# Performance work log

Measured on AMD Instinct MI355X. Metric: run time of the kernel, lower is better.

The kernel has to match this reference:

```python
import jax, jax.numpy as jnp
import numpy as np

# ---- static lookup-point config (matches cfg.radius/stride/level) ----
RADIUS = [4, 4, 4, 4]
STRIDE = [1, 1, 1, 1]
LEVEL = [0, 1, 2, 3]

def _build_pts():
    pts = {}
    for r, s, l in zip(RADIUS, STRIDE, LEVEL):
        pts.setdefault(l, set())
        for x in range(-r, r + 1):
            for y in range(-r, r + 1):
                pts[l].add((x * s, y * s))
    # sorted() reproduces torch's `v.sort()` on (x, y) tuples
    return {l: np.array(sorted(v), dtype=np.float32) for l, v in sorted(pts.items())}

PTS = _build_pts()                       # {lvl: (n_lvl, 2) offsets in level pixels}
N_LEVELS = max(LEVEL) + 1                # 4
CORR_DIM = 2 * sum(len(v) for v in PTS.values())   # 648
C_HALF = CORR_DIM // 2                   # 324 = per-direction channels
B, C, H, W = 1, 256, 80, 80


def _bilinear_sample(corr, x, y):
    """corr: (B, P, h, w); x, y: (P, n) pixel coords (align_corners=False convention,
    already converted to pixel space). Zero padding outside. Returns (B, P, n)."""
    Bn, P, h, w = corr.shape
    cf = corr.reshape(Bn, P, h * w)
    x0 = jnp.floor(x)
    y0 = jnp.floor(y)
    wx1 = x - x0
    wy1 = y - y0
    x0i = x0.astype(jnp.int32)
    y0i = y0.astype(jnp.int32)
    out = jnp.zeros((Bn, P, x.shape[-1]), corr.dtype)
    for dx, wxx in ((0, 1.0 - wx1), (1, wx1)):
        for dy, wyy in ((0, 1.0 - wy1), (1, wy1)):
            xi = x0i + dx
            yi = y0i + dy
            valid = (xi >= 0) & (xi < w) & (yi >= 0) & (yi < h)
            idx = jnp.clip(yi, 0, h - 1) * w + jnp.clip(xi, 0, w - 1)   # (P, n)
            v = jnp.take_along_axis(cf, jnp.broadcast_to(idx[None], (Bn,) + idx.shape), axis=2)
            out = out + v * (wxx * wyy * valid)[None]
    return out


def _lookup_pyramid(pyr):
    """pyr[lvl]: (B, P, H>>lvl, W>>lvl). Returns (B, P, C_HALF)."""
    outs = []
    for lvl, pts in PTS.items():
        s = 1 << lvl
        n = pts.shape[0]
        dxy = jnp.asarray(pts)
        # grid_sample align_corners=False: level-pixel coord of full-res pixel j is
        # (2j+1)/(2s) - 0.5; neighbor offsets are exactly `pts` in level pixels.
        bx = (2.0 * jnp.arange(W) + 1.0) / (2.0 * s) - 0.5   # (W,)
        by = (2.0 * jnp.arange(H) + 1.0) / (2.0 * s) - 0.5   # (H,)
        x = jnp.broadcast_to(bx[None, :, None] + dxy[None, None, :, 0], (H, W, n)).reshape(H * W, n)
        y = jnp.broadcast_to(by[:, None, None] + dxy[None, None, :, 1], (H, W, n)).reshape(H * W, n)
        outs.append(_bilinear_sample(pyr[lvl], x, y))
    return jnp.concatenate(outs, axis=-1)


def _pyramid(corr):
    """corr: (B, P, H, W) -> list of avg-pooled levels (2x2, stride 2)."""
    p = [corr]
    for _ in range(N_LEVELS - 1):
        b, pp, h, w = corr.shape
        corr = corr.reshape(b, pp, h // 2, 2, w // 2, 2).mean(axis=(3, 5))
        p.append(corr)
    return p


def _conv3x3_relu(x, w, b):
    y = jax.lax.conv_general_dilated(x, w, (1, 1), 'SAME',
                                     dimension_numbers=('NHWC', 'HWIO', 'NHWC'))
    return jax.nn.relu(y + b)


def _layer_norm(x, g, b, eps=1e-5):
    m = x.mean(-1, keepdims=True)
    v = ((x - m) ** 2).mean(-1, keepdims=True)
    return (x - m) * jax.lax.rsqrt(v + eps) * g + b


def setup_inputs() -> dict:
    key = jax.random.key(0)
    ks = jax.random.split(key, 4)
    return {
        'f0': jax.random.normal(ks[0], (B, C, H, W), jnp.float32),
        'f1': jax.random.normal(ks[1], (B, C, H, W), jnp.float32),
        'conv_w1': jax.random.normal(ks[2], (3, 3, C_HALF, C_HALF), jnp.float32) * 0.02,
        'conv_b1': jnp.zeros((C_HALF,), jnp.float32),
        'conv_w2': jax.random.normal(ks[3], (3, 3, C_HALF, C_HALF), jnp.float32) * 0.02,
        'conv_b2': jnp.zeros((C_HALF,), jnp.float32),
        'ln_g': jnp.ones((C_HALF,), jnp.float32),
        'ln_b': jnp.zeros((C_HALF,), jnp.float32),
    }


def reference(f0, f1, conv_w1, conv_b1, conv_w2, conv_b2, ln_g, ln_b):
    Bn, Cn, Hn, Wn = f0.shape
    P = Hn * Wn
    a = f0.reshape(Bn, Cn, P)
    bb = f1.reshape(Bn, Cn, P)
    corr01 = jnp.einsum('bcp,bcq->bpq', a, bb)          # (B, P, P)
    corr10 = jnp.swapaxes(corr01, 1, 2)
    feat01 = _lookup_pyramid(_pyramid(corr01.reshape(Bn, P, Hn, Wn)))   # (B, P, C_HALF)
    feat10 = _lookup_pyramid(_pyramid(corr10.reshape(Bn, P, Hn, Wn)))

    def branch(feat):
        x = feat.reshape(Bn, Hn, Wn, C_HALF)
        y = x + _conv3x3_relu(_conv3x3_relu(x, conv_w1, conv_b1), conv_w2, conv_b2)
        y = _layer_norm(y, ln_g, ln_b)
        return jnp.transpose(y, (0, 3, 1, 2))           # (B, C_HALF, H, W)

    return jnp.concatenate([branch(feat01), branch(feat10)], axis=1)    # (B, 2*C_HALF, H, W)
```

## Files before the change

### kernel.cpp

```cpp
#include <hip/hip_runtime.h>

typedef unsigned short u16;
typedef unsigned int   u32;
typedef float f32x4 __attribute__((ext_vector_type(4)));
typedef __bf16 bf16x8 __attribute__((ext_vector_type(8)));
typedef unsigned short u16x8 __attribute__((ext_vector_type(8)));
typedef unsigned short u16x4 __attribute__((ext_vector_type(4)));

#define PP   6400
#define HH   80
#define WW   80
#define KC   256
#define CH   324
#define CPAD 384
#define PW   82
#define PPIX (PW*PW)
#define NP2  896

__device__ inline float b2f(u16 u) { union { u32 i; float f; } v; v.i = ((u32)u) << 16; return v.f; }
__device__ inline u16 f2b(float f) {
    union { u32 i; float f; } v; v.f = f;
    u32 r = v.i + 0x7fffu + ((v.i >> 16) & 1u);
    return (u16)(r >> 16);
}

__device__ __forceinline__ void gload16(const void* g, void* l) {
    __builtin_amdgcn_global_load_lds((const __attribute__((address_space(1))) void*)g,
                                     (__attribute__((address_space(3))) void*)l, 16, 0, 0);
}

__global__ __launch_bounds__(256) void prep_f(const float* __restrict__ f0,
                                              const float* __restrict__ f1,
                                              u16* __restrict__ fA, u16* __restrict__ fB) {
    __shared__ float tile[64][65];
    int p0 = blockIdx.x * 64, c0 = blockIdx.y * 64;
    const float* src = blockIdx.z ? f1 : f0;
    u16* dst = blockIdx.z ? fB : fA;
    int tid = threadIdx.x;
#pragma unroll
    for (int it = 0; it < 4; ++it) {
        int idx = tid + it * 256;
        int cc = idx >> 4, pp4 = (idx & 15) * 4;
        f32x4 v = *(const f32x4*)(&src[(size_t)(c0 + cc) * PP + p0 + pp4]);
        tile[cc][pp4]     = v[0];
        tile[cc][pp4 + 1] = v[1];
        tile[cc][pp4 + 2] = v[2];
        tile[cc][pp4 + 3] = v[3];
    }
    __syncthreads();
#pragma unroll
    for (int it = 0; it < 4; ++it) {
        int idx = tid + it * 256;
        int pp = idx >> 4, cc4 = (idx & 15) * 4;
        u16x4 o;
        o[0] = f2b(tile[cc4][pp]);
        o[1] = f2b(tile[cc4 + 1][pp]);
        o[2] = f2b(tile[cc4 + 2][pp]);
        o[3] = f2b(tile[cc4 + 3][pp]);
        *(u16x4*)(&dst[(size_t)(p0 + pp) * KC + c0 + cc4]) = o;
    }
}

__global__ __launch_bounds__(256) void prep_w(const float* __restrict__ w1,
                                              const float* __restrict__ w2,
                                              u16* __restrict__ wT1, u16* __restrict__ wT2) {
    __shared__ float tile[64][65];
    int tap = blockIdx.x;
    int t6 = blockIdx.y;
    int ci0 = (t6 / 6) * 64, co0 = (t6 % 6) * 64;
    const float* w = blockIdx.z ? w2 : w1;
    u16* wT = blockIdx.z ? wT2 : wT1;
    int tid = threadIdx.x;
#pragma unroll
    for (int it = 0; it < 16; ++it) {
        int idx = tid + it * 256;
        int ciL = idx >> 6, coL = idx & 63;
        int ci = ci0 + ciL, co = co0 + coL;
        tile[ciL][coL] = (ci < CH && co < CH) ? w[((size_t)tap * CH + ci) * CH + co] : 0.f;
    }
    __syncthreads();
#pragma unroll
    for (int it = 0; it < 16; ++it) {
        int idx = tid + it * 256;
        int coL = idx >> 6, ciL = idx & 63;
        wT[((size_t)tap * CPAD + co0 + coL) * CPAD + ci0 + ciL] = f2b(tile[ciL][coL]);
    }
}

__global__ __launch_bounds__(384) void zero_border(u16* __restrict__ feat, u16* __restrict__ t1,
                                                   const float* __restrict__ b1,
                                                   const float* __restrict__ b2,
                                                   float* __restrict__ b1p, float* __restrict__ b2p) {
    int bi = blockIdx.x, dir = blockIdx.y;
    int t = threadIdx.x;
    if (bi == 324) {
        if (dir == 0) b1p[t] = t < CH ? b1[t] : 0.f;
        else          b2p[t] = t < CH ? b2[t] : 0.f;
        return;
    }
    int pix;
    if (bi < 82) pix = bi;
    else if (bi < 164) pix = 81 * PW + (bi - 82);
    else if (bi < 244) pix = (bi - 164 + 1) * PW;
    else pix = (bi - 244 + 1) * PW + 81;
    size_t off = ((size_t)dir * PPIX + pix) * CPAD + t;
    feat[off] = 0;
    t1[off] = 0;
}

__global__ __launch_bounds__(256) void pool_feat(const u16* __restrict__ fA,
                                                 const u16* __restrict__ fB,
                                                 u16* __restrict__ pbarA,
                                                 u16* __restrict__ pbarB) {
    int j = blockIdx.x;
    const u16* src = blockIdx.y ? fA : fB;
    u16* dst = blockIdx.y ? pbarA : pbarB;
    int k = threadIdx.x;
    int cy3 = j / 10, cx3 = j % 10;
    float l1v[16], l2v[4];
#pragma unroll
    for (int a = 0; a < 4; ++a)
#pragma unroll
        for (int b = 0; b < 4; ++b) {
            int cy = cy3 * 4 + a, cx = cx3 * 4 + b;
            int p00 = (2 * cy) * 80 + 2 * cx;
            float v = 0.25f * (b2f(src[(size_t)p00 * KC + k]) + b2f(src[(size_t)(p00 + 1) * KC + k]) +
                               b2f(src[(size_t)(p00 + 80) * KC + k]) + b2f(src[(size_t)(p00 + 81) * KC + k]));
            l1v[a * 4 + b] = v;
            dst[(size_t)(cy * 40 + cx) * KC + k] = f2b(v);
        }
#pragma unroll
    for (int a = 0; a < 2; ++a)
#pragma unroll
        for (int b = 0; b < 2; ++b) {
            float v = 0.25f * (l1v[(2 * a) * 4 + 2 * b] + l1v[(2 * a) * 4 + 2 * b + 1] +
                               l1v[(2 * a + 1) * 4 + 2 * b] + l1v[(2 * a + 1) * 4 + 2 * b + 1]);
            l2v[a * 2 + b] = v;
            dst[(size_t)(1600 + (cy3 * 2 + a) * 20 + cx3 * 2 + b) * KC + k] = f2b(v);
        }
    float v3 = 0.25f * (l2v[0] + l2v[1] + l2v[2] + l2v[3]);
    dst[(size_t)(2000 + j) * KC + k] = f2b(v3);
}

__global__ __launch_bounds__(256) void gemm_cp(const u16* __restrict__ fA,
                                               const u16* __restrict__ fB,
                                               const u16* __restrict__ pbarA,
                                               const u16* __restrict__ pbarB,
                                               u16* __restrict__ pc,
                                               u16* __restrict__ feat) {
    int y = blockIdx.y;
    bool band = (y < 7);
    int m0 = blockIdx.x * 128, n0 = 0, jbase = 0, dir = 0;
    const u16 *Aptr, *Bptr;
    if (band) {
        int n0t = (int)blockIdx.x + y - 3;
        if (n0t < 0 || n0t >= 50) return;
        n0 = n0t * 128;
        Aptr = fA; Bptr = fB;
    } else {
        int q = y - 7;
        dir = q / 7;
        jbase = (q % 7) * 128;
        Aptr = dir ? fB : fA;
        Bptr = dir ? pbarA : pbarB;
    }
    int py0 = m0 / 80;
    int s1 = min(max(py0 / 2 - 5, 0), 28);
    int s2 = min(max(py0 / 4 - 5, 0), 8);

    __shared__ __align__(16) char smem[128 * 136 * 2];
    u16* As = (u16*)smem;
    u16* Bs = As + 128 * 64;
    u16* trans = (u16*)smem;
    const int TS = 136;
    int tid = threadIdx.x;
    int wave = tid >> 6, lane = tid & 63;
    int quad = lane >> 4, l16 = lane & 15;
    int lrow = lane >> 3, lchunk = lane & 7;
    int sc = lchunk ^ (lrow & 7);
    int sw = l16 & 7;
    int wr = (wave >> 1) * 64, wc = (wave & 1) * 64;
    f32x4 acc[4][4] = {};

    size_t gRow[4];
#pragma unroll
    for (int i = 0; i < 4; ++i) {
        int row = i * 32 + wave * 8 + lrow;
        if (band) gRow[i] = (size_t)(n0 + row);
        else {
            int j = jbase + row;
            int g = j < 480 ? s1 * 40 + j
                  : j < 720 ? 1120 + s2 * 20 + j
                  : j < 820 ? 1280 + j
                  : 2099;
            gRow[i] = (size_t)g;
        }
    }

    for (int k0 = 0; k0 < KC; k0 += 64) {
        __syncthreads();
#pragma unroll
        for (int i = 0; i < 4; ++i) {
            int row = i * 32 + wave * 8 + lrow;
            gload16(&Aptr[(size_t)(m0 + row) * KC + k0 + sc * 8], &As[(i * 32 + wave * 8) * 64]);
            gload16(&Bptr[gRow[i] * KC + k0 + sc * 8], &Bs[(i * 32 + wave * 8) * 64]);
        }
        __syncthreads();
#pragma unroll
        for (int ki = 0; ki < 2; ++ki) {
            bf16x8 af[4], bfr[4];
#pragma unroll
            for (int mi = 0; mi < 4; ++mi) {
                int r = wr + mi * 16 + l16;
                af[mi] = *(const bf16x8*)(&As[r * 64 + (((ki * 4 + quad) ^ sw) * 8)]);
            }
#pragma unroll
            for (int ni = 0; ni < 4; ++ni) {
                int r = wc + ni * 16 + l16;
                bfr[ni] = *(const bf16x8*)(&Bs[r * 64 + (((ki * 4 + quad) ^ sw) * 8)]);
            }
#pragma unroll
            for (int mi = 0; mi < 4; ++mi)
#pragma unroll
                for (int ni = 0; ni < 4; ++ni)
                    acc[mi][ni] = __builtin_amdgcn_mfma_f32_16x16x32_bf16(af[mi], bfr[ni], acc[mi][ni], 0, 0, 0);
        }
    }
    if (band) {
        u16* fd0 = feat;
        u16* fd1 = feat + (size_t)PPIX * CPAD;
#pragma unroll
        for (int ni = 0; ni < 4; ++ni) {
            int q = n0 + wc + ni * 16 + l16;
            int qy = q / 80, qx = q - qy * 80;
            size_t qpix = (size_t)((qy + 1) * PW + qx + 1) * CPAD;
#pragma unroll
            for (int mi = 0; mi < 4; ++mi)
#pragma unroll
                for (int rr = 0; rr < 4; ++rr) {
                    int p = m0 + wr + mi * 16 + quad * 4 + rr;
                    int py = p / 80, px = p - py * 80;
                    int dx = qx - px, dy = qy - py;
                    if ((unsigned)(dx + 4) < 9u && (unsigned)(dy + 4) < 9u) {
                        u16 v = f2b(acc[mi][ni][rr]);
                        size_t ppix = (size_t)((py + 1) * PW + px + 1) * CPAD;
                        fd0[ppix + (dx + 4) * 9 + (dy + 4)] = v;
                        fd1[qpix + (4 - dx) * 9 + (4 - dy)] = v;
                    }
                }
        }
        return;
    }
    __syncthreads();
#pragma unroll
    for (int mi = 0; mi < 4; ++mi)
#pragma unroll
        for (int ni = 0; ni < 4; ++ni) {
            int rbase = wr + mi * 16 + quad * 4;
            int c = wc + ni * 16 + l16;
#pragma unroll
            for (int rr = 0; rr < 4; ++rr)
                trans[(rbase + rr) * TS + c] = f2b(acc[mi][ni][rr]);
        }
    __syncthreads();
#pragma unroll
    for (int it = 0; it < 8; ++it) {
        int r = it * 16 + (tid >> 4);
        int c8 = (tid & 15) * 8;
        u16x8 v = *(const u16x8*)(&trans[r * TS + c8]);
        *(u16x8*)(&pc[((size_t)dir * PP + m0 + r) * NP2 + jbase + c8]) = v;
    }
}

__global__ __launch_bounds__(384) void lookup(const u16* __restrict__ pc,
                                              u16* __restrict__ feat) {
    __shared__ __align__(16) u16 pcrow[4][NP2];
    int p0 = blockIdx.x * 4, dir = blockIdx.y;
    int tid = threadIdx.x;
    int mt = p0 >> 7;
    int py0 = (mt * 128) / 80;
    int s1 = min(max(py0 / 2 - 5, 0), 28);
    int s2 = min(max(py0 / 4 - 5, 0), 8);
    for (int i = tid; i < 4 * (NP2 / 8); i += 384) {
        int j = i / (NP2 / 8), cc = i % (NP2 / 8);
        *(u16x8*)(&pcrow[j][cc * 8]) =
            *(const u16x8*)(&pc[((size_t)dir * PP + p0 + j) * NP2 + cc * 8]);
    }
    __syncthreads();
    int ch = tid;
#pragma unroll
    for (int j = 0; j < 4; ++j) {
        int p = p0 + j;
        int px = p % WW, py = p / WW;
        size_t pix = (size_t)(py + 1) * PW + px + 1;
        if (ch < 81) {
            int dx = ch / 9 - 4, dy = ch % 9 - 4;
            int x = px + dx, yy = py + dy;
            if ((unsigned)x >= (unsigned)WW || (unsigned)yy >= (unsigned)HH)
                feat[((size_t)dir * PPIX + pix) * CPAD + ch] = 0;
        } else if (ch < CH) {
            int lvl = ch / 81, i = ch % 81;
            int dx = i / 9 - 4, dy = i % 9 - 4;
            int wl = WW >> lvl;
            float inv = 1.0f / (float)(2 << lvl);
            float xc = (float)(2 * px + 1) * inv - 0.5f + (float)dx;
            float yc = (float)(2 * py + 1) * inv - 0.5f + (float)dy;
            float x0f = floorf(xc), y0f = floorf(yc);
            int x0 = (int)x0f, y0 = (int)y0f;
            float wx = xc - x0f, wy = yc - y0f;
            float val = 0.f;
#pragma unroll
            for (int cy = 0; cy < 2; ++cy)
#pragma unroll
                for (int cx = 0; cx < 2; ++cx) {
                    int xi = x0 + cx, yi = y0 + cy;
                    if ((unsigned)xi < (unsigned)wl && (unsigned)yi < (unsigned)wl) {
                        float wgt = (cx ? wx : 1.f - wx) * (cy ? wy : 1.f - wy);
                        int idx = (lvl == 1) ? (yi - s1) * 40 + xi
                                : (lvl == 2) ? 480 + (yi - s2) * 20 + xi
                                             : 720 + yi * 10 + xi;
                        val += b2f(pcrow[j][idx]) * wgt;
                    }
                }
            feat[((size_t)dir * PPIX + pix) * CPAD + ch] = f2b(val);
        } else {
            feat[((size_t)dir * PPIX + pix) * CPAD + ch] = 0;
        }
    }
}

__global__ __launch_bounds__(256) void conv_gemm(const u16* __restrict__ inFeat,
                                                 const u16* __restrict__ wTt,
                                                 const float* __restrict__ bias,
                                                 const u16* __restrict__ resid,
                                                 u16* __restrict__ outb) {
    int L = (int)blockIdx.x;
    int xcd = L & 7;
    int q = L >> 3;
    int n_t = q % 3; q /= 3;
    int mg = q % 13;
    int dir = q / 13;
    int m_t = mg * 8 + xcd;
    if (m_t >= 100) return;
    const u16* Ain = inFeat + (size_t)dir * PPIX * CPAD;
    const u16* Rin = resid ? resid + (size_t)dir * PPIX * CPAD : (const u16*)0;
    u16* Out = outb + (size_t)dir * PPIX * CPAD;
    __shared__ __align__(16) u16 As[64 * 128];
    __shared__ __align__(16) u16 Bs[128 * 128];
    int tid = threadIdx.x;
    int wave = tid >> 6, lane = tid & 63;
    int quad = lane >> 4, l16 = lane & 15;
    int wr = (wave >> 1) * 32, wc = (wave & 1) * 64;
    int m0 = m_t * 64, n0 = n_t * 128;
    f32x4 acc[2][4] = {};

    int pixA[4], scI[4];
#pragma unroll
    for (int i = 0; i < 4; ++i) {
        int r = wave * 16 + i * 4 + quad;
        int m = m0 + r;
        pixA[i] = (m / 80 + 1) * PW + (m % 80) + 1;
        scI[i] = l16 ^ ((i * 4 + quad) & 15);
    }

    for (int tap = 0; tap < 9; ++tap) {
        int dpix = (tap / 3 - 1) * PW + (tap % 3) - 1;
        const u16* Wt = wTt + ((size_t)tap * CPAD + n0) * CPAD;
#pragma unroll
        for (int kt = 0; kt < 3; ++kt) {
            int kc = kt * 128;
            __syncthreads();
#pragma unroll
            for (int i = 0; i < 4; ++i)
                gload16(&Ain[(size_t)(pixA[i] + dpix) * CPAD + kc + scI[i] * 8],
                        &As[(wave * 16 + i * 4) * 128]);
#pragma unroll
            for (int j = 0; j < 8; ++j) {
                int rb = wave * 32 + j * 4;
                gload16(&Wt[(size_t)(rb + quad) * CPAD + kc + scI[j & 3] * 8],
                        &Bs[rb * 128]);
            }
            __syncthreads();
#pragma unroll
            for (int ki = 0; ki < 4; ++ki) {
                int slot = (ki * 4 + quad) ^ l16;
                bf16x8 af[2], bfr[4];
#pragma unroll
                for (int mi = 0; mi < 2; ++mi)
                    af[mi] = *(const bf16x8*)(&As[(wr + mi * 16 + l16) * 128 + slot * 8]);
#pragma unroll
                for (int ni = 0; ni < 4; ++ni)
                    bfr[ni] = *(const bf16x8*)(&Bs[(wc + ni * 16 + l16) * 128 + slot * 8]);
#pragma unroll
                for (int mi = 0; mi < 2; ++mi)
#pragma unroll
                    for (int ni = 0; ni < 4; ++ni)
                        acc[mi][ni] = __builtin_amdgcn_mfma_f32_16x16x32_bf16(af[mi], bfr[ni], acc[mi][ni], 0, 0, 0);
            }
        }
    }
#pragma unroll
    for (int mi = 0; mi < 2; ++mi)
#pragma unroll
        for (int rr = 0; rr < 4; ++rr) {
            int p = m0 + wr + mi * 16 + quad * 4 + rr;
            size_t opix = (size_t)(p / 80 + 1) * PW + (p % 80) + 1;
#pragma unroll
            for (int ni = 0; ni < 4; ++ni) {
                int co = n0 + wc + ni * 16 + l16;
                float v = acc[mi][ni][rr] + bias[co];
                v = fmaxf(v, 0.f);
                if (Rin) v += b2f(Rin[opix * CPAD + co]);
                Out[opix * CPAD + co] = f2b(v);
            }
        }
}

__global__ __launch_bounds__(256) void ln_out(const u16* __restrict__ t2,
                                              const float* __restrict__ g,
                                              const float* __restrict__ b,
                                              float* __restrict__ out) {
    int dir = blockIdx.y;
    int p0 = blockIdx.x * 64;
    const u16* Y = t2 + (size_t)dir * PPIX * CPAD;
    __shared__ u16 buf[64 * 325];
    __shared__ float mean_s[64], inv_s[64];
    __shared__ float part[64][4][2];
    int tid = threadIdx.x;
    for (int ci = tid; ci < 64 * 40; ci += 256) {
        int pp = ci / 40, c8 = (ci - pp * 40) * 8;
        int p = p0 + pp;
        size_t pix = (size_t)(p / 80 + 1) * PW + (p % 80) + 1;
        u16x8 v = *(const u16x8*)(&Y[pix * CPAD + c8]);
#pragma unroll
        for (int k = 0; k < 8; ++k) buf[pp * 325 + c8 + k] = v[k];
    }
    {
        int pp = tid >> 2, k = tid & 3;
        int p = p0 + pp;
        size_t pix = (size_t)(p / 80 + 1) * PW + (p % 80) + 1;
        buf[pp * 325 + 320 + k] = Y[pix * CPAD + 320 + k];
    }
    __syncthreads();
    {
        int pp = tid >> 2, q = tid & 3;
        float s = 0.f, s2 = 0.f;
        for (int c = q; c < CH; c += 4) { float v = b2f(buf[pp * 325 + c]); s += v; s2 += v * v; }
        part[pp][q][0] = s; part[pp][q][1] = s2;
    }
    __syncthreads();
    if (tid < 64) {
        float s = 0.f, s2 = 0.f;
        for (int q = 0; q < 4; ++q) { s += part[tid][q][0]; s2 += part[tid][q][1]; }
        float m = s / (float)CH;
        float var = s2 / (float)CH - m * m;
        if (var < 0.f) var = 0.f;
        mean_s[tid] = m;
        inv_s[tid] = rsqrtf(var + 1e-5f);
    }
    __syncthreads();
    for (int idx = tid; idx < CH * 64; idx += 256) {
        int c = idx >> 6, pp = idx & 63;
        float v = (b2f(buf[pp * 325 + c]) - mean_s[pp]) * inv_s[pp] * g[c] + b[c];
        out[((size_t)(dir * CH + c)) * PP + p0 + pp] = v;
    }
}

extern "C" void kernel_launch(void* const* d_in, const int* in_sizes, int n_in,
                              void* d_out, int out_size, void* d_ws, size_t ws_size,
                              hipStream_t stream) {
    const float* f0  = (const float*)d_in[0];
    const float* f1  = (const float*)d_in[1];
    const float* w1  = (const float*)d_in[2];
    const float* b1  = (const float*)d_in[3];
    const float* w2  = (const float*)d_in[4];
    const float* b2  = (const float*)d_in[5];
    const float* lng = (const float*)d_in[6];
    const float* lnb = (const float*)d_in[7];
    float* out = (float*)d_out;

    char* ws = (char*)d_ws;
    size_t off = 0;
    auto alloc = [&](size_t bytes) -> char* {
        char* r = ws + off;
        off += (bytes + 511) & ~(size_t)511;
        return r;
    };
    u16* fA     = (u16*)alloc((size_t)PP * KC * 2);
    u16* fB     = (u16*)alloc((size_t)PP * KC * 2);
    u16* pc     = (u16*)alloc((size_t)2 * PP * NP2 * 2);
    u16* feat   = (u16*)alloc((size_t)2 * PPIX * CPAD * 2);
    u16* t1     = (u16*)alloc((size_t)2 * PPIX * CPAD * 2);
    u16* t2     = (u16*)alloc((size_t)2 * PPIX * CPAD * 2);
    u16* pbarA  = (u16*)alloc((size_t)2176 * KC * 2);
    u16* pbarB  = (u16*)alloc((size_t)2176 * KC * 2);
    u16* wT1    = (u16*)alloc((size_t)9 * CPAD * CPAD * 2);
    u16* wT2    = (u16*)alloc((size_t)9 * CPAD * CPAD * 2);
    float* b1p  = (float*)alloc(CPAD * 4);
    float* b2p  = (float*)alloc(CPAD * 4);

    prep_f<<<dim3(100, 4, 2), 256, 0, stream>>>(f0, f1, fA, fB);
    prep_w<<<dim3(9, 36, 2), 256, 0, stream>>>(w1, w2, wT1, wT2);
    zero_border<<<dim3(325, 2), 384, 0, stream>>>(feat, t1, b1, b2, b1p, b2p);
    pool_feat<<<dim3(100, 2), 256, 0, stream>>>(fA, fB, pbarA, pbarB);
    gemm_cp<<<dim3(50, 21), 256, 0, stream>>>(fA, fB, pbarA, pbarB, pc, feat);
    lookup<<<dim3(1600, 2), 384, 0, stream>>>(pc, feat);
    conv_gemm<<<dim3(624), 256, 0, stream>>>(feat, wT1, b1p, (const u16*)0, t1);
    conv_gemm<<<dim3(624), 256, 0, stream>>>(t1, wT2, b2p, feat, t2);
    ln_out<<<dim3(100, 2), 256, 0, stream>>>(t2, lng, lnb, out);
}
```

Measured before the change: 243.6 us.

## Merge prep kernels into two launches and widen GEMM K-tile to 128

```diff
diff --git a/kernel.cpp b/kernel.cpp
--- a/kernel.cpp
+++ b/kernel.cpp
@@ -29,114 +29,117 @@
                                      (__attribute__((address_space(3))) void*)l, 16, 0, 0);
 }
 
-__global__ __launch_bounds__(256) void prep_f(const float* __restrict__ f0,
-                                              const float* __restrict__ f1,
-                                              u16* __restrict__ fA, u16* __restrict__ fB) {
+__global__ __launch_bounds__(256) void prep_all(const float* __restrict__ f0,
+                                                const float* __restrict__ f1,
+                                                u16* __restrict__ fA, u16* __restrict__ fB,
+                                                const float* __restrict__ w1,
+                                                const float* __restrict__ w2,
+                                                u16* __restrict__ wT1, u16* __restrict__ wT2) {
     __shared__ float tile[64][65];
-    int p0 = blockIdx.x * 64, c0 = blockIdx.y * 64;
-    const float* src = blockIdx.z ? f1 : f0;
-    u16* dst = blockIdx.z ? fB : fA;
+    int bid = (int)blockIdx.x;
     int tid = threadIdx.x;
-#pragma unroll
-    for (int it = 0; it < 4; ++it) {
-        int idx = tid + it * 256;
-        int cc = idx >> 4, pp4 = (idx & 15) * 4;
-        f32x4 v = *(const f32x4*)(&src[(size_t)(c0 + cc) * PP + p0 + pp4]);
-        tile[cc][pp4]     = v[0];
-        tile[cc][pp4 + 1] = v[1];
-        tile[cc][pp4 + 2] = v[2];
-        tile[cc][pp4 + 3] = v[3];
-    }
-    __syncthreads();
-#pragma unroll
-    for (int it = 0; it < 4; ++it) {
-        int idx = tid + it * 256;
-        int pp = idx >> 4, cc4 = (idx & 15) * 4;
-        u16x4 o;
-        o[0] = f2b(tile[cc4][pp]);
-        o[1] = f2b(tile[cc4 + 1][pp]);
-        o[2] = f2b(tile[cc4 + 2][pp]);
-        o[3] = f2b(tile[cc4 + 3][pp]);
-        *(u16x4*)(&dst[(size_t)(p0 + pp) * KC + c0 + cc4]) = o;
-    }
-}
-
-__global__ __launch_bounds__(256) void prep_w(const float* __restrict__ w1,
-                                              const float* __restrict__ w2,
-                                              u16* __restrict__ wT1, u16* __restrict__ wT2) {
-    __shared__ float tile[64][65];
-    int tap = blockIdx.x;
-    int t6 = blockIdx.y;
-    int ci0 = (t6 / 6) * 64, co0 = (t6 % 6) * 64;
-    const float* w = blockIdx.z ? w2 : w1;
-    u16* wT = blockIdx.z ? wT2 : wT1;
-    int tid = threadIdx.x;
-#pragma unroll
-    for (int it = 0; it < 16; ++it) {
-        int idx = tid + it * 256;
-        int ciL = idx >> 6, coL = idx & 63;
-        int ci = ci0 + ciL, co = co0 + coL;
-        tile[ciL][coL] = (ci < CH && co < CH) ? w[((size_t)tap * CH + ci) * CH + co] : 0.f;
-    }
-    __syncthreads();
-#pragma unroll
-    for (int it = 0; it < 16; ++it) {
-        int idx = tid + it * 256;
-        int coL = idx >> 6, ciL = idx & 63;
-        wT[((size_t)tap * CPAD + co0 + coL) * CPAD + ci0 + ciL] = f2b(tile[ciL][coL]);
-    }
-}
-
-__global__ __launch_bounds__(384) void zero_border(u16* __restrict__ feat, u16* __restrict__ t1,
-                                                   const float* __restrict__ b1,
-                                                   const float* __restrict__ b2,
-                                                   float* __restrict__ b1p, float* __restrict__ b2p) {
-    int bi = blockIdx.x, dir = blockIdx.y;
+    if (bid < 800) {
+        int x = bid % 100, yb = (bid / 100) % 4, z = bid / 400;
+        int p0 = x * 64, c0 = yb * 64;
+        const float* src = z ? f1 : f0;
+        u16* dst = z ? fB : fA;
+#pragma unroll
+        for (int it = 0; it < 4; ++it) {
+            int idx = tid + it * 256;
+            int cc = idx >> 4, pp4 = (idx & 15) * 4;
+            f32x4 v = *(const f32x4*)(&src[(size_t)(c0 + cc) * PP + p0 + pp4]);
+            tile[cc][pp4]     = v[0];
+            tile[cc][pp4 + 1] = v[1];
+            tile[cc][pp4 + 2] = v[2];
+            tile[cc][pp4 + 3] = v[3];
+        }
+        __syncthreads();
+#pragma unroll
+        for (int it = 0; it < 4; ++it) {
+            int idx = tid + it * 256;
+            int pp = idx >> 4, cc4 = (idx & 15) * 4;
+            u16x4 o;
+            o[0] = f2b(tile[cc4][pp]);
+            o[1] = f2b(tile[cc4 + 1][pp]);
+            o[2] = f2b(tile[cc4 + 2][pp]);
+            o[3] = f2b(tile[cc4 + 3][pp]);
+            *(u16x4*)(&dst[(size_t)(p0 + pp) * KC + c0 + cc4]) = o;
+        }
+    } else {
+        int b = bid - 800;
+        int tap = b % 9, t6 = (b / 9) % 36, z = b / 324;
+        int ci0 = (t6 / 6) * 64, co0 = (t6 % 6) * 64;
+        const float* w = z ? w2 : w1;
+        u16* wT = z ? wT2 : wT1;
+#pragma unroll
+        for (int it = 0; it < 16; ++it) {
+            int idx = tid + it * 256;
+            int ciL = idx >> 6, coL = idx & 63;
+            int ci = ci0 + ciL, co = co0 + coL;
+            tile[ciL][coL] = (ci < CH && co < CH) ? w[((size_t)tap * CH + ci) * CH + co] : 0.f;
+        }
+        __syncthreads();
+#pragma unroll
+        for (int it = 0; it < 16; ++it) {
+            int idx = tid + it * 256;
+            int coL = idx >> 6, ciL = idx & 63;
+            wT[((size_t)tap * CPAD + co0 + coL) * CPAD + ci0 + ciL] = f2b(tile[ciL][coL]);
+        }
+    }
+}
+
+__global__ __launch_bounds__(384) void zpool(u16* __restrict__ feat, u16* __restrict__ t1,
+                                             const float* __restrict__ b1,
+                                             const float* __restrict__ b2,
+                                             float* __restrict__ b1p, float* __restrict__ b2p,
+                                             const u16* __restrict__ fA, const u16* __restrict__ fB,
+                                             u16* __restrict__ pbarA, u16* __restrict__ pbarB) {
+    int bid = (int)blockIdx.x;
     int t = threadIdx.x;
-    if (bi == 324) {
-        if (dir == 0) b1p[t] = t < CH ? b1[t] : 0.f;
-        else          b2p[t] = t < CH ? b2[t] : 0.f;
+    if (bid < 650) {
+        int bi = bid % 325, dir = bid / 325;
+        if (bi == 324) {
+            if (dir == 0) b1p[t] = t < CH ? b1[t] : 0.f;
+            else          b2p[t] = t < CH ? b2[t] : 0.f;
+            return;
+        }
+        int pix;
+        if (bi < 82) pix = bi;
+        else if (bi < 164) pix = 81 * PW + (bi - 82);
+        else if (bi < 244) pix = (bi - 164 + 1) * PW;
+        else pix = (bi - 244 + 1) * PW + 81;
+        size_t off = ((size_t)dir * PPIX + pix) * CPAD + t;
+        feat[off] = 0;
+        t1[off] = 0;
         return;
     }
-    int pix;
-    if (bi < 82) pix = bi;
-    else if (bi < 164) pix = 81 * PW + (bi - 82);
-    else if (bi < 244) pix = (bi - 164 + 1) * PW;
-    else pix = (bi - 244 + 1) * PW + 81;
-    size_t off = ((size_t)dir * PPIX + pix) * CPAD + t;
-    feat[off] = 0;
-    t1[off] = 0;
-}
-
-__global__ __launch_bounds__(256) void pool_feat(const u16* __restrict__ fA,
-                                                 const u16* __restrict__ fB,
-                                                 u16* __restrict__ pbarA,
-                                                 u16* __restrict__ pbarB) {
-    int j = blockIdx.x;
-    const u16* src = blockIdx.y ? fA : fB;
-    u16* dst = blockIdx.y ? pbarA : pbarB;
-    int k = threadIdx.x;
+    if (t >= 256) return;
+    int b = bid - 650;
+    int j = b % 100, yy = b / 100;
+    const u16* src = yy ? fA : fB;
+    u16* dst = yy ? pbarA : pbarB;
+    int k = t;
     int cy3 = j / 10, cx3 = j % 10;
     float l1v[16], l2v[4];
 #pragma unroll
     for (int a = 0; a < 4; ++a)
 #pragma unroll
-        for (int b = 0; b < 4; ++b) {
-            int cy = cy3 * 4 + a, cx = cx3 * 4 + b;
+        for (int bb = 0; bb < 4; ++bb) {
+            int cy = cy3 * 4 + a, cx = cx3 * 4 + bb;
             int p00 = (2 * cy) * 80 + 2 * cx;
             float v = 0.25f * (b2f(src[(size_t)p00 * KC + k]) + b2f(src[(size_t)(p00 + 1) * KC + k]) +
                                b2f(src[(size_t)(p00 + 80) * KC + k]) + b2f(src[(size_t)(p00 + 81) * KC + k]));
-            l1v[a * 4 + b] = v;
+            l1v[a * 4 + bb] = v;
             dst[(size_t)(cy * 40 + cx) * KC + k] = f2b(v);
         }
 #pragma unroll
     for (int a = 0; a < 2; ++a)
 #pragma unroll
-        for (int b = 0; b < 2; ++b) {
-            float v = 0.25f * (l1v[(2 * a) * 4 + 2 * b] + l1v[(2 * a) * 4 + 2 * b + 1] +
-                               l1v[(2 * a + 1) * 4 + 2 * b] + l1v[(2 * a + 1) * 4 + 2 * b + 1]);
-            l2v[a * 2 + b] = v;
-            dst[(size_t)(1600 + (cy3 * 2 + a) * 20 + cx3 * 2 + b) * KC + k] = f2b(v);
+        for (int bb = 0; bb < 2; ++bb) {
+            float v = 0.25f * (l1v[(2 * a) * 4 + 2 * bb] + l1v[(2 * a) * 4 + 2 * bb + 1] +
+                               l1v[(2 * a + 1) * 4 + 2 * bb] + l1v[(2 * a + 1) * 4 + 2 * bb + 1]);
+            l2v[a * 2 + bb] = v;
+            dst[(size_t)(1600 + (cy3 * 2 + a) * 20 + cx3 * 2 + bb) * KC + k] = f2b(v);
         }
     float v3 = 0.25f * (l2v[0] + l2v[1] + l2v[2] + l2v[3]);
     dst[(size_t)(2000 + j) * KC + k] = f2b(v3);
@@ -168,24 +171,24 @@
     int s1 = min(max(py0 / 2 - 5, 0), 28);
     int s2 = min(max(py0 / 4 - 5, 0), 8);
 
-    __shared__ __align__(16) char smem[128 * 136 * 2];
+    __shared__ __align__(16) char smem[65536];
     u16* As = (u16*)smem;
-    u16* Bs = As + 128 * 64;
+    u16* Bs = As + 128 * 128;
     u16* trans = (u16*)smem;
     const int TS = 136;
     int tid = threadIdx.x;
     int wave = tid >> 6, lane = tid & 63;
     int quad = lane >> 4, l16 = lane & 15;
-    int lrow = lane >> 3, lchunk = lane & 7;
-    int sc = lchunk ^ (lrow & 7);
-    int sw = l16 & 7;
     int wr = (wave >> 1) * 64, wc = (wave & 1) * 64;
     f32x4 acc[4][4] = {};
 
-    size_t gRow[4];
-#pragma unroll
-    for (int i = 0; i < 4; ++i) {
-        int row = i * 32 + wave * 8 + lrow;
+    int aRow[8], scW[8];
+    size_t gRow[8];
+#pragma unroll
+    for (int i = 0; i < 8; ++i) {
+        int row = wave * 32 + i * 4 + quad;
+        aRow[i] = m0 + row;
+        scW[i] = l16 ^ (row & 15);
         if (band) gRow[i] = (size_t)(n0 + row);
         else {
             int j = jbase + row;
@@ -197,28 +200,27 @@
         }
     }
 
-    for (int k0 = 0; k0 < KC; k0 += 64) {
+#pragma unroll
+    for (int k0 = 0; k0 < 2; ++k0) {
+        int kc = k0 * 128;
         __syncthreads();
 #pragma unroll
-        for (int i = 0; i < 4; ++i) {
-            int row = i * 32 + wave * 8 + lrow;
-            gload16(&Aptr[(size_t)(m0 + row) * KC + k0 + sc * 8], &As[(i * 32 + wave * 8) * 64]);
-            gload16(&Bptr[gRow[i] * KC + k0 + sc * 8], &Bs[(i * 32 + wave * 8) * 64]);
-        }
+        for (int i = 0; i < 8; ++i)
+            gload16(&Aptr[(size_t)aRow[i] * KC + kc + scW[i] * 8], &As[(wave * 32 + i * 4) * 128]);
+#pragma unroll
+        for (int j = 0; j < 8; ++j)
+            gload16(&Bptr[gRow[j] * KC + kc + scW[j] * 8], &Bs[(wave * 32 + j * 4) * 128]);
         __syncthreads();
 #pragma unroll
-        for (int ki = 0; ki < 2; ++ki) {
+        for (int ki = 0; ki < 4; ++ki) {
+            int slot = (ki * 4 + quad) ^ l16;
             bf16x8 af[4], bfr[4];
 #pragma unroll
-            for (int mi = 0; mi < 4; ++mi) {
-                int r = wr + mi * 16 + l16;
-                af[mi] = *(const bf16x8*)(&As[r * 64 + (((ki * 4 + quad) ^ sw) * 8)]);
-            }
-#pragma unroll
-            for (int ni = 0; ni < 4; ++ni) {
-                int r = wc + ni * 16 + l16;
-                bfr[ni] = *(const bf16x8*)(&Bs[r * 64 + (((ki * 4 + quad) ^ sw) * 8)]);
-            }
+            for (int mi = 0; mi < 4; ++mi)
+                af[mi] = *(const bf16x8*)(&As[(wr + mi * 16 + l16) * 128 + slot * 8]);
+#pragma unroll
+            for (int ni = 0; ni < 4; ++ni)
+                bfr[ni] = *(const bf16x8*)(&Bs[(wc + ni * 16 + l16) * 128 + slot * 8]);
 #pragma unroll
             for (int mi = 0; mi < 4; ++mi)
 #pragma unroll
@@ -499,10 +501,8 @@
     float* b1p  = (float*)alloc(CPAD * 4);
     float* b2p  = (float*)alloc(CPAD * 4);
 
-    prep_f<<<dim3(100, 4, 2), 256, 0, stream>>>(f0, f1, fA, fB);
-    prep_w<<<dim3(9, 36, 2), 256, 0, stream>>>(w1, w2, wT1, wT2);
-    zero_border<<<dim3(325, 2), 384, 0, stream>>>(feat, t1, b1, b2, b1p, b2p);
-    pool_feat<<<dim3(100, 2), 256, 0, stream>>>(fA, fB, pbarA, pbarB);
+    prep_all<<<dim3(1448), 256, 0, stream>>>(f0, f1, fA, fB, w1, w2, wT1, wT2);
+    zpool<<<dim3(850), 384, 0, stream>>>(feat, t1, b1, b2, b1p, b2p, fA, fB, pbarA, pbarB);
     gemm_cp<<<dim3(50, 21), 256, 0, stream>>>(fA, fB, pbarA, pbarB, pc, feat);
     lookup<<<dim3(1600, 2), 384, 0, stream>>>(pc, feat);
     conv_gemm<<<dim3(624), 256, 0, stream>>>(feat, wT1, b1p, (const u16*)0, t1);
```

New measurement: 245.2 us. Within noise of the previous version (+0.7%).
